# Kernel optimization log

Measured on AMD Instinct MI355X. Metric: run time of the kernel, lower is better.

The kernel has to match this reference:

```python
import jax, jax.numpy as jnp
import numpy as np

D_MODEL = 1024
NUM_HEADS = 16
KEY_DIM = 64
VALUE_DIM = 64
NEG_INF = jnp.float32(-1e30)


def setup_inputs() -> dict:
    key = jax.random.key(0)
    ks = jax.random.split(key, 10)
    B, S = 2, 2048
    lim = 1.0 / np.sqrt(D_MODEL)
    x = jax.random.normal(ks[0], (B, S, D_MODEL), dtype=jnp.float32)
    mask = jnp.ones((B, S), dtype=jnp.int32)  # pad mask: 1 = keep
    # stacked per-head linear params (Linear stores weight as [out, in])
    Wq = jax.random.uniform(ks[1], (NUM_HEADS, KEY_DIM, D_MODEL), jnp.float32, -lim, lim)
    bq = jax.random.uniform(ks[2], (NUM_HEADS, KEY_DIM), jnp.float32, -lim, lim)
    Wk = jax.random.uniform(ks[3], (NUM_HEADS, KEY_DIM, D_MODEL), jnp.float32, -lim, lim)
    bk = jax.random.uniform(ks[4], (NUM_HEADS, KEY_DIM), jnp.float32, -lim, lim)
    Wv = jax.random.uniform(ks[5], (NUM_HEADS, VALUE_DIM, D_MODEL), jnp.float32, -lim, lim)
    bv = jax.random.uniform(ks[6], (NUM_HEADS, VALUE_DIM), jnp.float32, -lim, lim)
    lim_o = 1.0 / np.sqrt(NUM_HEADS * VALUE_DIM)
    Wo = jax.random.uniform(ks[7], (D_MODEL, NUM_HEADS * VALUE_DIM), jnp.float32, -lim_o, lim_o)
    bo = jax.random.uniform(ks[8], (D_MODEL,), jnp.float32, -lim_o, lim_o)
    return {"x": x, "mask": mask, "Wq": Wq, "bq": bq, "Wk": Wk, "bk": bk,
            "Wv": Wv, "bv": bv, "Wo": Wo, "bo": bo}


def _mha(x, mask, Wq, bq, Wk, bk, Wv, bv, Wo, bo):
    B, S, _ = x.shape
    # per-head projections: [B, H, S, k]
    q = jnp.einsum('bsd,hkd->bhsk', x, Wq) + bq[None, :, None, :]
    k = jnp.einsum('bsd,hkd->bhsk', x, Wk) + bk[None, :, None, :]
    v = jnp.einsum('bsd,hvd->bhsv', x, Wv) + bv[None, :, None, :]
    scale = 1.0 / np.sqrt(KEY_DIM).astype(np.float32)
    scores = jnp.einsum('bhik,bhjk->bhij', q, k) * scale  # [B, H, S, S]
    # final mask = causal AND pad-row AND pad-col
    causal = jnp.tril(jnp.ones((S, S), dtype=bool))
    pad = mask.astype(bool)
    final = causal[None, None] & pad[:, None, :, None] & pad[:, None, None, :]
    masked = jnp.where(final, scores, NEG_INF)
    w = jax.nn.softmax(masked, axis=-1)
    w = jnp.where(final, w, 0.0)  # fully-masked rows -> zeros, matching loop impl
    out = jnp.einsum('bhij,bhjv->bhiv', w, v)            # [B, H, S, V]
    concat = out.transpose(0, 2, 1, 3).reshape(B, S, NUM_HEADS * VALUE_DIM)
    return concat @ Wo.T + bo


def reference(x, mask, Wq, bq, Wk, bk, Wv, bv, Wo, bo):
    return _mha(x, mask, Wq, bq, Wk, bk, Wv, bv, Wo, bo)
```

## Files before the change

kernel.cpp:

```cpp
#include <hip/hip_runtime.h>

#define SEQ 2048
#define NH 16
#define HD 64
#define DMODEL 1024

__device__ __forceinline__ unsigned int f2bf(float f) {
  unsigned int u = __float_as_uint(f);
  return ((u + 0x7fffu + ((u >> 16) & 1u)) >> 16) & 0xffffu;
}

__device__ __forceinline__ unsigned int pk2bf(float a, float b) {
  unsigned short ua = __builtin_bit_cast(unsigned short, (__bf16)a);
  unsigned short ub = __builtin_bit_cast(unsigned short, (__bf16)b);
  return (unsigned int)ua | ((unsigned int)ub << 16);
}

typedef __bf16 bf16x8 __attribute__((ext_vector_type(8)));
typedef float f32x4 __attribute__((ext_vector_type(4)));
typedef unsigned int uix4 __attribute__((ext_vector_type(4)));
typedef unsigned int uix2 __attribute__((ext_vector_type(2)));

__device__ __forceinline__ void gl2lds16(const unsigned short* g, unsigned short* l) {
  __builtin_amdgcn_global_load_lds(
      (const __attribute__((address_space(1))) unsigned int*)g,
      (__attribute__((address_space(3))) unsigned int*)l, 16, 0, 0);
}

__global__ __launch_bounds__(256) void cast_all_kernel(
    const float* __restrict__ x, const float* __restrict__ wq,
    const float* __restrict__ wk, const float* __restrict__ wv,
    const float* __restrict__ wo,
    unsigned short* __restrict__ xb, unsigned short* __restrict__ wqb,
    unsigned short* __restrict__ wkb, unsigned short* __restrict__ wvb,
    unsigned short* __restrict__ wob) {
  int idx = blockIdx.x * 256 + threadIdx.x;
  if (idx >= 1048576) return;
  const float* src;
  unsigned short* dst;
  int off;
  if (idx < 524288) {
    src = x; dst = xb; off = idx;
  } else {
    int t = idx - 524288;
    int w = t >> 17;
    off = t & 131071;
    src = (w == 0) ? wq : (w == 1) ? wk : (w == 2) ? wv : wo;
    dst = (w == 0) ? wqb : (w == 1) ? wkb : (w == 2) ? wvb : wob;
  }
  const float4* p = reinterpret_cast<const float4*>(src) + (size_t)off * 2;
  float4 a = p[0], b = p[1];
  uint4 o;
  o.x = f2bf(a.x) | (f2bf(a.y) << 16);
  o.y = f2bf(a.z) | (f2bf(a.w) << 16);
  o.z = f2bf(b.x) | (f2bf(b.y) << 16);
  o.w = f2bf(b.z) | (f2bf(b.w) << 16);
  reinterpret_cast<uint4*>(dst)[off] = o;
}

template <int MODE, int TM>
__global__ __launch_bounds__(256) void gemm128(
    const unsigned short* __restrict__ A, const unsigned short* __restrict__ B,
    const float* __restrict__ bias0, const float* __restrict__ bias1,
    const float* __restrict__ bias2, float* __restrict__ Cf,
    unsigned short* __restrict__ Qo, unsigned short* __restrict__ Ko,
    unsigned short* __restrict__ Vto, int Kdim) {
  constexpr int MT = TM / 32;
  __shared__ __align__(16) unsigned short As[2][TM * 64];
  __shared__ __align__(16) unsigned short Bs[2][128 * 64];
  const int tid = threadIdx.x;
  const int wave = tid >> 6, lane = tid & 63;
  const int wm = wave >> 1, wn = wave & 1;
  const int fr = lane & 15, quad = lane >> 4;
  const int fx = fr & 7;
  const int n0 = blockIdx.x * 128, m0 = blockIdx.y * TM;

  const int srowg = lane >> 3;
  const int schunk = (lane & 7) ^ (srowg & 7);
  const unsigned short* Abase =
      A + (size_t)(m0 + wave * (TM / 4) + srowg) * Kdim + schunk * 8;
  const unsigned short* Bbase =
      B + (size_t)(n0 + wave * 32 + srowg) * Kdim + schunk * 8;
  const int awoff = (wave * (TM / 4)) * 64;
  const int bwoff = (wave * 32) * 64;

  f32x4 acc[MT][4];
#pragma unroll
  for (int mt = 0; mt < MT; ++mt)
#pragma unroll
    for (int nt = 0; nt < 4; ++nt) acc[mt][nt] = f32x4{0.f, 0.f, 0.f, 0.f};

#pragma unroll
  for (int t = 0; t < TM / 32; ++t)
    gl2lds16(Abase + (size_t)(t * 8) * Kdim, As[0] + awoff + t * 8 * 64);
#pragma unroll
  for (int t = 0; t < 4; ++t)
    gl2lds16(Bbase + (size_t)(t * 8) * Kdim, Bs[0] + bwoff + t * 8 * 64);

  const int nk = Kdim >> 6;
  for (int kk = 0; kk < nk; ++kk) {
    __syncthreads();
    if (kk + 1 < nk) {
      const int k0n = (kk + 1) * 64;
      unsigned short* An = As[(kk + 1) & 1] + awoff;
      unsigned short* Bn = Bs[(kk + 1) & 1] + bwoff;
#pragma unroll
      for (int t = 0; t < TM / 32; ++t)
        gl2lds16(Abase + (size_t)(t * 8) * Kdim + k0n, An + t * 8 * 64);
#pragma unroll
      for (int t = 0; t < 4; ++t)
        gl2lds16(Bbase + (size_t)(t * 8) * Kdim + k0n, Bn + t * 8 * 64);
    }
    const unsigned short* Acur = As[kk & 1];
    const unsigned short* Bcur = Bs[kk & 1];
#pragma unroll
    for (int ks = 0; ks < 2; ++ks) {
      bf16x8 af[MT], bfv[4];
#pragma unroll
      for (int mt = 0; mt < MT; ++mt)
        af[mt] = *reinterpret_cast<const bf16x8*>(
            Acur + (wm * (TM / 2) + mt * 16 + fr) * 64 + ((ks * 4 + quad) ^ fx) * 8);
#pragma unroll
      for (int nt = 0; nt < 4; ++nt)
        bfv[nt] = *reinterpret_cast<const bf16x8*>(
            Bcur + (wn * 64 + nt * 16 + fr) * 64 + ((ks * 4 + quad) ^ fx) * 8);
#pragma unroll
      for (int mt = 0; mt < MT; ++mt)
#pragma unroll
        for (int nt = 0; nt < 4; ++nt)
          acc[mt][nt] = __builtin_amdgcn_mfma_f32_16x16x32_bf16(
              af[mt], bfv[nt], acc[mt][nt], 0, 0, 0);
    }
  }

  if (MODE == 0) {
    const int seg = n0 >> 10;
    const float* bp = (seg == 0) ? bias0 : (seg == 1) ? bias1 : bias2;
    const float scale = (seg == 0) ? 0.1803368809f : 1.0f;
    unsigned short* QK = (seg == 0) ? Qo : Ko;
#pragma unroll
    for (int nt = 0; nt < 4; ++nt) {
      const int c = (n0 + wn * 64 + nt * 16 + fr) & 1023;
      const int h = c >> 6, d = c & 63;
      const float bs = bp[c];
#pragma unroll
      for (int mt = 0; mt < MT; ++mt) {
        const int mbase = m0 + wm * (TM / 2) + mt * 16 + quad * 4;
        const int b = mbase >> 11, s0 = mbase & 2047;
        if (seg < 2) {
          unsigned short* dst = QK + (((size_t)(b * NH + h)) * SEQ + s0) * HD + d;
#pragma unroll
          for (int r = 0; r < 4; ++r)
            dst[(size_t)r * HD] = (unsigned short)f2bf((acc[mt][nt][r] + bs) * scale);
        } else {
          uint2 pk;
          pk.x = pk2bf(acc[mt][nt][0] + bs, acc[mt][nt][1] + bs);
          pk.y = pk2bf(acc[mt][nt][2] + bs, acc[mt][nt][3] + bs);
          *reinterpret_cast<uint2*>(
              Vto + (((size_t)(b * NH + h)) * HD + d) * SEQ + s0) = pk;
        }
      }
    }
  } else {
#pragma unroll
    for (int nt = 0; nt < 4; ++nt) {
      const int cg = n0 + wn * 64 + nt * 16 + fr;
      const float bs = bias0[cg];
#pragma unroll
      for (int mt = 0; mt < MT; ++mt) {
        const int mbase = m0 + wm * (TM / 2) + mt * 16 + quad * 4;
#pragma unroll
        for (int r = 0; r < 4; ++r)
          Cf[(size_t)(mbase + r) * DMODEL + cg] = acc[mt][nt][r] + bs;
      }
    }
  }
}

__global__ __launch_bounds__(256, 4) void attn_mfma_kernel(
    const unsigned short* __restrict__ Qg, const unsigned short* __restrict__ Kg,
    const unsigned short* __restrict__ Vtg, const int* __restrict__ mask,
    unsigned short* __restrict__ concat) {
  const int w = blockIdx.x >> 8;
  const int c = blockIdx.x & 255;
  const int gg = c >> 5;
  const int bh = c & 31;
  const int ib = (w == 0) ? (31 - gg) : (w == 1) ? gg : (w == 2) ? (23 - gg) : (8 + gg);
  const int b = bh >> 4, h = bh & 15;
  const int tid = threadIdx.x;
  const int wave = tid >> 6, lane = tid & 63;
  const int quad = lane >> 4, fr = lane & 15;
  const int fx = fr & 7;

  __shared__ __align__(16) unsigned short Ks[2][64 * 64];
  __shared__ __align__(16) unsigned short Vts[2][64 * 64];

  const unsigned short* Qb = Qg + ((size_t)bh * SEQ) * HD;
  const unsigned short* Kb = Kg + ((size_t)bh * SEQ) * HD;
  const unsigned short* Vtb = Vtg + ((size_t)bh * HD) * SEQ;
  const int* maskb = mask + b * SEQ;

  bool badl = false;
  {
    const int4* mp4 = reinterpret_cast<const int4*>(maskb);
#pragma unroll
    for (int u = 0; u < 8; ++u) {
      int4 v = mp4[lane * 8 + u];
      badl |= !(v.x && v.y && v.z && v.w);
    }
  }
  const unsigned long long bm = __ballot(badl);

  const int ir = ib * 64 + wave * 16 + fr;
  const bf16x8 q0 = *reinterpret_cast<const bf16x8*>(Qb + (size_t)ir * HD + quad * 8);
  const bf16x8 q1 = *reinterpret_cast<const bf16x8*>(Qb + (size_t)ir * HD + quad * 8 + 32);
  const int padi = maskb[ir];

  f32x4 o[4];
#pragma unroll
  for (int vt = 0; vt < 4; ++vt) o[vt] = f32x4{0.f, 0.f, 0.f, 0.f};
  float mr = -1e20f;
  float lq = 0.f;

  const int srow8 = lane >> 3;
  const int sch8 = (lane & 7) ^ (srow8 & 7);
  const int kprow = (wave >> 1) * 32 + ((srow8 >> 2)) * 8 + (wave & 1) * 4 + (srow8 & 3);
  const unsigned short* Kcol = Kb + sch8 * 8;
  const unsigned short* Vsrc = Vtb + (size_t)(wave * 16 + srow8) * SEQ + sch8 * 8;
  const int cA0 = (quad ^ fx) * 8;
  const int cA1 = ((quad + 4) ^ fx) * 8;

  {
    unsigned short* KsW = Ks[0] + (wave * 16) * 64;
    unsigned short* VtsW = Vts[0] + (wave * 16) * 64;
#pragma unroll
    for (int t = 0; t < 2; ++t) {
      gl2lds16(Kcol + (size_t)(kprow + t * 16) * HD, KsW + t * 8 * 64);
      gl2lds16(Vsrc + (size_t)(t * 8) * SEQ, VtsW + t * 8 * 64);
    }
  }

  for (int jc = 0; jc <= ib; ++jc) {
    __syncthreads();
    if (jc < ib) {
      const int jn = (jc + 1) * 64;
      unsigned short* KsW = Ks[(jc + 1) & 1] + (wave * 16) * 64;
      unsigned short* VtsW = Vts[(jc + 1) & 1] + (wave * 16) * 64;
#pragma unroll
      for (int t = 0; t < 2; ++t) {
        gl2lds16(Kcol + (size_t)(jn + kprow + t * 16) * HD, KsW + t * 8 * 64);
        gl2lds16(Vsrc + (size_t)(t * 8) * SEQ + jn, VtsW + t * 8 * 64);
      }
    }
    const unsigned short* Kcur = Ks[jc & 1];
    const unsigned short* Vcur = Vts[jc & 1];
    const int j0 = jc * 64;
    const bool tb = ((bm >> (2 * jc)) & 3ull) != 0ull;

    f32x4 st[4];
    __builtin_amdgcn_s_setprio(1);
#pragma unroll
    for (int jt = 0; jt < 4; ++jt) {
      bf16x8 ka0 = *reinterpret_cast<const bf16x8*>(&Kcur[(jt * 16 + fr) * 64 + cA0]);
      bf16x8 ka1 = *reinterpret_cast<const bf16x8*>(&Kcur[(jt * 16 + fr) * 64 + cA1]);
      st[jt] = f32x4{0.f, 0.f, 0.f, 0.f};
      st[jt] = __builtin_amdgcn_mfma_f32_16x16x32_bf16(ka0, q0, st[jt], 0, 0, 0);
      st[jt] = __builtin_amdgcn_mfma_f32_16x16x32_bf16(ka1, q1, st[jt], 0, 0, 0);
    }
    __builtin_amdgcn_s_setprio(0);

    if (tb) {
      const int4* mp = reinterpret_cast<const int4*>(maskb + j0);
#pragma unroll
      for (int jt = 0; jt < 4; ++jt) {
        const int4 mv = mp[(jt >> 1) * 8 + quad * 2 + (jt & 1)];
        if (mv.x == 0) st[jt][0] = -1e30f;
        if (mv.y == 0) st[jt][1] = -1e30f;
        if (mv.z == 0) st[jt][2] = -1e30f;
        if (mv.w == 0) st[jt][3] = -1e30f;
      }
    }
    if (jc == ib) {
#pragma unroll
      for (int jt = 0; jt < 4; ++jt) {
        const int jb = j0 + (jt >> 1) * 32 + quad * 8 + (jt & 1) * 4;
#pragma unroll
        for (int r = 0; r < 4; ++r)
          if (jb + r > ir) st[jt][r] = -1e30f;
      }
    }

    float tmax = -1e30f;
#pragma unroll
    for (int jt = 0; jt < 4; ++jt)
#pragma unroll
      for (int r = 0; r < 4; ++r) tmax = fmaxf(tmax, st[jt][r]);
    tmax = fmaxf(tmax, __shfl_xor(tmax, 16));
    {
      uix2 rr = __builtin_amdgcn_permlane32_swap(__float_as_uint(tmax),
                                                 __float_as_uint(tmax), false, false);
      tmax = fmaxf(__uint_as_float(rr.x), __uint_as_float(rr.y));
    }
    if (jc == 0) mr = fmaxf(tmax, -1e20f);

    unsigned int pw[8];
#pragma unroll
    for (int jt = 0; jt < 4; ++jt) {
      float p0 = __builtin_amdgcn_exp2f(fminf(st[jt][0] - mr, 60.f));
      float p1 = __builtin_amdgcn_exp2f(fminf(st[jt][1] - mr, 60.f));
      float p2 = __builtin_amdgcn_exp2f(fminf(st[jt][2] - mr, 60.f));
      float p3 = __builtin_amdgcn_exp2f(fminf(st[jt][3] - mr, 60.f));
      lq += (p0 + p1) + (p2 + p3);
      pw[2 * jt] = pk2bf(p0, p1);
      pw[2 * jt + 1] = pk2bf(p2, p3);
    }
    const bf16x8 pa0 = __builtin_bit_cast(bf16x8, uix4{pw[0], pw[1], pw[2], pw[3]});
    const bf16x8 pa1 = __builtin_bit_cast(bf16x8, uix4{pw[4], pw[5], pw[6], pw[7]});

    __builtin_amdgcn_s_setprio(1);
#pragma unroll
    for (int vt = 0; vt < 4; ++vt) {
      bf16x8 vb0 = *reinterpret_cast<const bf16x8*>(&Vcur[(vt * 16 + fr) * 64 + cA0]);
      bf16x8 vb1 = *reinterpret_cast<const bf16x8*>(&Vcur[(vt * 16 + fr) * 64 + cA1]);
      o[vt] = __builtin_amdgcn_mfma_f32_16x16x32_bf16(vb0, pa0, o[vt], 0, 0, 0);
      o[vt] = __builtin_amdgcn_mfma_f32_16x16x32_bf16(vb1, pa1, o[vt], 0, 0, 0);
    }
    __builtin_amdgcn_s_setprio(0);

    if (jc > 0) {
      const bool upd = __ballot(tmax > mr + 8.f) != 0ull;
      if (upd) {
        const float mn = fmaxf(mr, tmax);
        const float corr = __builtin_amdgcn_exp2f(mr - mn);
        mr = mn;
        lq *= corr;
#pragma unroll
        for (int vt = 0; vt < 4; ++vt) {
          o[vt][0] *= corr; o[vt][1] *= corr; o[vt][2] *= corr; o[vt][3] *= corr;
        }
      }
    }
  }

  float lr = lq;
  lr += __shfl_xor(lr, 16);
  lr += __shfl_xor(lr, 32);
  const float inv = (padi != 0 && lr > 0.f) ? 1.f / lr : 0.f;
  unsigned short* orow = concat + ((size_t)(b * SEQ + ir)) * DMODEL + h * HD;
#pragma unroll
  for (int vt = 0; vt < 4; ++vt) {
    uint2 pk;
    pk.x = pk2bf(o[vt][0] * inv, o[vt][1] * inv);
    pk.y = pk2bf(o[vt][2] * inv, o[vt][3] * inv);
    *reinterpret_cast<uint2*>(orow + vt * 16 + quad * 4) = pk;
  }
}

extern "C" void kernel_launch(void* const* d_in, const int* in_sizes, int n_in,
                              void* d_out, int out_size, void* d_ws, size_t ws_size,
                              hipStream_t stream) {
  (void)in_sizes; (void)n_in; (void)out_size;
  const float* x  = (const float*)d_in[0];
  const int* mask = (const int*)d_in[1];
  const float* Wq = (const float*)d_in[2];
  const float* bq = (const float*)d_in[3];
  const float* Wk = (const float*)d_in[4];
  const float* bk = (const float*)d_in[5];
  const float* Wv = (const float*)d_in[6];
  const float* bv = (const float*)d_in[7];
  const float* Wo = (const float*)d_in[8];
  const float* bo = (const float*)d_in[9];
  float* out = (float*)d_out;

  char* ws = (char*)d_ws;
  if (ws_size < (48ull << 20)) return;
  unsigned short* xb  = (unsigned short*)(ws);
  unsigned short* wqb = (unsigned short*)(ws + (8ull  << 20));
  unsigned short* wkb = (unsigned short*)(ws + (10ull << 20));
  unsigned short* wvb = (unsigned short*)(ws + (12ull << 20));
  unsigned short* wob = (unsigned short*)(ws + (14ull << 20));
  unsigned short* Qb  = (unsigned short*)(ws + (16ull << 20));
  unsigned short* Kb  = (unsigned short*)(ws + (24ull << 20));
  unsigned short* Vtb = (unsigned short*)(ws + (32ull << 20));
  unsigned short* cb  = (unsigned short*)(ws + (40ull << 20));

  cast_all_kernel<<<4096, 256, 0, stream>>>(x, Wq, Wk, Wv, Wo, xb, wqb, wkb, wvb, wob);

  gemm128<0, 128><<<dim3(24, 32), 256, 0, stream>>>(xb, wqb, bq, bk, bv,
                                                    nullptr, Qb, Kb, Vtb, 1024);

  attn_mfma_kernel<<<1024, 256, 0, stream>>>(Qb, Kb, Vtb, mask, cb);

  gemm128<1, 64><<<dim3(8, 64), 256, 0, stream>>>(cb, wob, bo, nullptr, nullptr,
                                                  out, nullptr, nullptr, nullptr, 1024);
}
```

Baseline: 192.6 us.

## Process two 16-row query tiles per wave in attention with 128-thread blocks

The attention kernel now uses 2 waves per block instead of 4, and each wave handles 32 query rows as two 16-row tiles. Every K and V fragment read from LDS therefore feeds two MFMAs. Each wave also issues twice as many global-to-LDS loads to fill the same 64x64 tiles. This cuts LDS read traffic per MFMA and gives each wave more independent work. The cost is roughly double the register use per wave for accumulators and scores, fewer waves per block, and a rescale that now triggers for both row tiles whenever either one needs it.

Result: slower. 204.7 us (+6.3%).

```diff
diff --git a/kernel.cpp b/kernel.cpp
--- a/kernel.cpp
+++ b/kernel.cpp
@@ -177,7 +177,7 @@
   }
 }
 
-__global__ __launch_bounds__(256, 4) void attn_mfma_kernel(
+__global__ __launch_bounds__(128, 3) void attn_mfma_kernel(
     const unsigned short* __restrict__ Qg, const unsigned short* __restrict__ Kg,
     const unsigned short* __restrict__ Vtg, const int* __restrict__ mask,
     unsigned short* __restrict__ concat) {
@@ -211,45 +211,49 @@
   }
   const unsigned long long bm = __ballot(badl);
 
-  const int ir = ib * 64 + wave * 16 + fr;
-  const bf16x8 q0 = *reinterpret_cast<const bf16x8*>(Qb + (size_t)ir * HD + quad * 8);
-  const bf16x8 q1 = *reinterpret_cast<const bf16x8*>(Qb + (size_t)ir * HD + quad * 8 + 32);
-  const int padi = maskb[ir];
-
-  f32x4 o[4];
-#pragma unroll
-  for (int vt = 0; vt < 4; ++vt) o[vt] = f32x4{0.f, 0.f, 0.f, 0.f};
-  float mr = -1e20f;
-  float lq = 0.f;
-
-  const int srow8 = lane >> 3;
-  const int sch8 = (lane & 7) ^ (srow8 & 7);
-  const int kprow = (wave >> 1) * 32 + ((srow8 >> 2)) * 8 + (wave & 1) * 4 + (srow8 & 3);
-  const unsigned short* Kcol = Kb + sch8 * 8;
-  const unsigned short* Vsrc = Vtb + (size_t)(wave * 16 + srow8) * SEQ + sch8 * 8;
+  int ir[2], padi[2];
+  bf16x8 q[2][2];
+#pragma unroll
+  for (int it = 0; it < 2; ++it) {
+    ir[it] = ib * 64 + wave * 32 + it * 16 + fr;
+    q[it][0] = *reinterpret_cast<const bf16x8*>(Qb + (size_t)ir[it] * HD + quad * 8);
+    q[it][1] = *reinterpret_cast<const bf16x8*>(Qb + (size_t)ir[it] * HD + quad * 8 + 32);
+    padi[it] = maskb[ir[it]];
+  }
+
+  f32x4 o[2][4];
+#pragma unroll
+  for (int it = 0; it < 2; ++it)
+#pragma unroll
+    for (int vt = 0; vt < 4; ++vt) o[it][vt] = f32x4{0.f, 0.f, 0.f, 0.f};
+  float mr[2] = {-1e20f, -1e20f};
+  float lq[2] = {0.f, 0.f};
+
+  const int sr = lane >> 3;
+  const int sch = (lane & 7) ^ (sr & 7);
+  const unsigned short* Kcol = Kb + sch * 8;
+  const unsigned short* Vsrc = Vtb + (size_t)(wave * 32 + sr) * SEQ + sch * 8;
   const int cA0 = (quad ^ fx) * 8;
   const int cA1 = ((quad + 4) ^ fx) * 8;
 
-  {
-    unsigned short* KsW = Ks[0] + (wave * 16) * 64;
-    unsigned short* VtsW = Vts[0] + (wave * 16) * 64;
-#pragma unroll
-    for (int t = 0; t < 2; ++t) {
-      gl2lds16(Kcol + (size_t)(kprow + t * 16) * HD, KsW + t * 8 * 64);
-      gl2lds16(Vsrc + (size_t)(t * 8) * SEQ, VtsW + t * 8 * 64);
-    }
+#pragma unroll
+  for (int t = 0; t < 4; ++t) {
+    const int kp = wave * 32 + ((t & 1) << 4) + ((sr >> 2) << 3) + ((t >> 1) << 2) + (sr & 3);
+    gl2lds16(Kcol + (size_t)kp * HD, Ks[0] + (wave * 32 + t * 8) * 64);
+    gl2lds16(Vsrc + (size_t)(t * 8) * SEQ, Vts[0] + (wave * 32 + t * 8) * 64);
   }
 
   for (int jc = 0; jc <= ib; ++jc) {
     __syncthreads();
     if (jc < ib) {
       const int jn = (jc + 1) * 64;
-      unsigned short* KsW = Ks[(jc + 1) & 1] + (wave * 16) * 64;
-      unsigned short* VtsW = Vts[(jc + 1) & 1] + (wave * 16) * 64;
-#pragma unroll
-      for (int t = 0; t < 2; ++t) {
-        gl2lds16(Kcol + (size_t)(jn + kprow + t * 16) * HD, KsW + t * 8 * 64);
-        gl2lds16(Vsrc + (size_t)(t * 8) * SEQ + jn, VtsW + t * 8 * 64);
+      unsigned short* Ksn = Ks[(jc + 1) & 1];
+      unsigned short* Vtsn = Vts[(jc + 1) & 1];
+#pragma unroll
+      for (int t = 0; t < 4; ++t) {
+        const int kp = wave * 32 + ((t & 1) << 4) + ((sr >> 2) << 3) + ((t >> 1) << 2) + (sr & 3);
+        gl2lds16(Kcol + (size_t)(jn + kp) * HD, Ksn + (wave * 32 + t * 8) * 64);
+        gl2lds16(Vsrc + (size_t)(t * 8) * SEQ + jn, Vtsn + (wave * 32 + t * 8) * 64);
       }
     }
     const unsigned short* Kcur = Ks[jc & 1];
@@ -257,15 +261,18 @@
     const int j0 = jc * 64;
     const bool tb = ((bm >> (2 * jc)) & 3ull) != 0ull;
 
-    f32x4 st[4];
+    f32x4 st[2][4];
     __builtin_amdgcn_s_setprio(1);
 #pragma unroll
     for (int jt = 0; jt < 4; ++jt) {
       bf16x8 ka0 = *reinterpret_cast<const bf16x8*>(&Kcur[(jt * 16 + fr) * 64 + cA0]);
       bf16x8 ka1 = *reinterpret_cast<const bf16x8*>(&Kcur[(jt * 16 + fr) * 64 + cA1]);
-      st[jt] = f32x4{0.f, 0.f, 0.f, 0.f};
-      st[jt] = __builtin_amdgcn_mfma_f32_16x16x32_bf16(ka0, q0, st[jt], 0, 0, 0);
-      st[jt] = __builtin_amdgcn_mfma_f32_16x16x32_bf16(ka1, q1, st[jt], 0, 0, 0);
+#pragma unroll
+      for (int it = 0; it < 2; ++it) {
+        st[it][jt] = f32x4{0.f, 0.f, 0.f, 0.f};
+        st[it][jt] = __builtin_amdgcn_mfma_f32_16x16x32_bf16(ka0, q[it][0], st[it][jt], 0, 0, 0);
+        st[it][jt] = __builtin_amdgcn_mfma_f32_16x16x32_bf16(ka1, q[it][1], st[it][jt], 0, 0, 0);
+      }
     }
     __builtin_amdgcn_s_setprio(0);
 
@@ -274,10 +281,13 @@
 #pragma unroll
       for (int jt = 0; jt < 4; ++jt) {
         const int4 mv = mp[(jt >> 1) * 8 + quad * 2 + (jt & 1)];
-        if (mv.x == 0) st[jt][0] = -1e30f;
-        if (mv.y == 0) st[jt][1] = -1e30f;
-        if (mv.z == 0) st[jt][2] = -1e30f;
-        if (mv.w == 0) st[jt][3] = -1e30f;
+#pragma unroll
+        for (int it = 0; it < 2; ++it) {
+          if (mv.x == 0) st[it][jt][0] = -1e30f;
+          if (mv.y == 0) st[it][jt][1] = -1e30f;
+          if (mv.z == 0) st[it][jt][2] = -1e30f;
+          if (mv.w == 0) st[it][jt][3] = -1e30f;
+        }
       }
     }
     if (jc == ib) {
@@ -285,74 +295,95 @@
       for (int jt = 0; jt < 4; ++jt) {
         const int jb = j0 + (jt >> 1) * 32 + quad * 8 + (jt & 1) * 4;
 #pragma unroll
-        for (int r = 0; r < 4; ++r)
-          if (jb + r > ir) st[jt][r] = -1e30f;
-      }
-    }
-
-    float tmax = -1e30f;
-#pragma unroll
-    for (int jt = 0; jt < 4; ++jt)
-#pragma unroll
-      for (int r = 0; r < 4; ++r) tmax = fmaxf(tmax, st[jt][r]);
-    tmax = fmaxf(tmax, __shfl_xor(tmax, 16));
-    {
-      uix2 rr = __builtin_amdgcn_permlane32_swap(__float_as_uint(tmax),
-                                                 __float_as_uint(tmax), false, false);
-      tmax = fmaxf(__uint_as_float(rr.x), __uint_as_float(rr.y));
-    }
-    if (jc == 0) mr = fmaxf(tmax, -1e20f);
-
-    unsigned int pw[8];
-#pragma unroll
-    for (int jt = 0; jt < 4; ++jt) {
-      float p0 = __builtin_amdgcn_exp2f(fminf(st[jt][0] - mr, 60.f));
-      float p1 = __builtin_amdgcn_exp2f(fminf(st[jt][1] - mr, 60.f));
-      float p2 = __builtin_amdgcn_exp2f(fminf(st[jt][2] - mr, 60.f));
-      float p3 = __builtin_amdgcn_exp2f(fminf(st[jt][3] - mr, 60.f));
-      lq += (p0 + p1) + (p2 + p3);
-      pw[2 * jt] = pk2bf(p0, p1);
-      pw[2 * jt + 1] = pk2bf(p2, p3);
-    }
-    const bf16x8 pa0 = __builtin_bit_cast(bf16x8, uix4{pw[0], pw[1], pw[2], pw[3]});
-    const bf16x8 pa1 = __builtin_bit_cast(bf16x8, uix4{pw[4], pw[5], pw[6], pw[7]});
+        for (int it = 0; it < 2; ++it)
+#pragma unroll
+          for (int r = 0; r < 4; ++r)
+            if (jb + r > ir[it]) st[it][jt][r] = -1e30f;
+      }
+    }
+
+    float tmax[2];
+#pragma unroll
+    for (int it = 0; it < 2; ++it) {
+      float t0 = -1e30f;
+#pragma unroll
+      for (int jt = 0; jt < 4; ++jt)
+#pragma unroll
+        for (int r = 0; r < 4; ++r) t0 = fmaxf(t0, st[it][jt][r]);
+      t0 = fmaxf(t0, __shfl_xor(t0, 16));
+      uix2 rr = __builtin_amdgcn_permlane32_swap(__float_as_uint(t0),
+                                                 __float_as_uint(t0), false, false);
+      tmax[it] = fmaxf(__uint_as_float(rr.x), __uint_as_float(rr.y));
+    }
+    if (jc == 0) {
+      mr[0] = fmaxf(tmax[0], -1e20f);
+      mr[1] = fmaxf(tmax[1], -1e20f);
+    }
+
+    bf16x8 pa[2][2];
+#pragma unroll
+    for (int it = 0; it < 2; ++it) {
+      unsigned int pw[8];
+#pragma unroll
+      for (int jt = 0; jt < 4; ++jt) {
+        float p0 = __builtin_amdgcn_exp2f(fminf(st[it][jt][0] - mr[it], 60.f));
+        float p1 = __builtin_amdgcn_exp2f(fminf(st[it][jt][1] - mr[it], 60.f));
+        float p2 = __builtin_amdgcn_exp2f(fminf(st[it][jt][2] - mr[it], 60.f));
+        float p3 = __builtin_amdgcn_exp2f(fminf(st[it][jt][3] - mr[it], 60.f));
+        lq[it] += (p0 + p1) + (p2 + p3);
+        pw[2 * jt] = pk2bf(p0, p1);
+        pw[2 * jt + 1] = pk2bf(p2, p3);
+      }
+      pa[it][0] = __builtin_bit_cast(bf16x8, uix4{pw[0], pw[1], pw[2], pw[3]});
+      pa[it][1] = __builtin_bit_cast(bf16x8, uix4{pw[4], pw[5], pw[6], pw[7]});
+    }
 
     __builtin_amdgcn_s_setprio(1);
 #pragma unroll
     for (int vt = 0; vt < 4; ++vt) {
       bf16x8 vb0 = *reinterpret_cast<const bf16x8*>(&Vcur[(vt * 16 + fr) * 64 + cA0]);
       bf16x8 vb1 = *reinterpret_cast<const bf16x8*>(&Vcur[(vt * 16 + fr) * 64 + cA1]);
-      o[vt] = __builtin_amdgcn_mfma_f32_16x16x32_bf16(vb0, pa0, o[vt], 0, 0, 0);
-      o[vt] = __builtin_amdgcn_mfma_f32_16x16x32_bf16(vb1, pa1, o[vt], 0, 0, 0);
+#pragma unroll
+      for (int it = 0; it < 2; ++it) {
+        o[it][vt] = __builtin_amdgcn_mfma_f32_16x16x32_bf16(vb0, pa[it][0], o[it][vt], 0, 0, 0);
+        o[it][vt] = __builtin_amdgcn_mfma_f32_16x16x32_bf16(vb1, pa[it][1], o[it][vt], 0, 0, 0);
+      }
     }
     __builtin_amdgcn_s_setprio(0);
 
     if (jc > 0) {
-      const bool upd = __ballot(tmax > mr + 8.f) != 0ull;
-      if (upd) {
-        const float mn = fmaxf(mr, tmax);
-        const float corr = __builtin_amdgcn_exp2f(mr - mn);
-        mr = mn;
-        lq *= corr;
-#pragma unroll
-        for (int vt = 0; vt < 4; ++vt) {
-          o[vt][0] *= corr; o[vt][1] *= corr; o[vt][2] *= corr; o[vt][3] *= corr;
+      const bool need = (tmax[0] > mr[0] + 8.f) || (tmax[1] > mr[1] + 8.f);
+      if (__ballot(need) != 0ull) {
+#pragma unroll
+        for (int it = 0; it < 2; ++it) {
+          const float mn = fmaxf(mr[it], tmax[it]);
+          const float corr = __builtin_amdgcn_exp2f(mr[it] - mn);
+          mr[it] = mn;
+          lq[it] *= corr;
+#pragma unroll
+          for (int vt = 0; vt < 4; ++vt) {
+            o[it][vt][0] *= corr; o[it][vt][1] *= corr;
+            o[it][vt][2] *= corr; o[it][vt][3] *= corr;
+          }
         }
       }
     }
   }
 
-  float lr = lq;
-  lr += __shfl_xor(lr, 16);
-  lr += __shfl_xor(lr, 32);
-  const float inv = (padi != 0 && lr > 0.f) ? 1.f / lr : 0.f;
-  unsigned short* orow = concat + ((size_t)(b * SEQ + ir)) * DMODEL + h * HD;
-#pragma unroll
-  for (int vt = 0; vt < 4; ++vt) {
-    uint2 pk;
-    pk.x = pk2bf(o[vt][0] * inv, o[vt][1] * inv);
-    pk.y = pk2bf(o[vt][2] * inv, o[vt][3] * inv);
-    *reinterpret_cast<uint2*>(orow + vt * 16 + quad * 4) = pk;
+#pragma unroll
+  for (int it = 0; it < 2; ++it) {
+    float lr = lq[it];
+    lr += __shfl_xor(lr, 16);
+    lr += __shfl_xor(lr, 32);
+    const float inv = (padi[it] != 0 && lr > 0.f) ? 1.f / lr : 0.f;
+    unsigned short* orow = concat + ((size_t)(b * SEQ + ir[it])) * DMODEL + h * HD;
+#pragma unroll
+    for (int vt = 0; vt < 4; ++vt) {
+      uint2 pk;
+      pk.x = pk2bf(o[it][vt][0] * inv, o[it][vt][1] * inv);
+      pk.y = pk2bf(o[it][vt][2] * inv, o[it][vt][3] * inv);
+      *reinterpret_cast<uint2*>(orow + vt * 16 + quad * 4) = pk;
+    }
   }
 }
 
@@ -389,7 +420,7 @@
   gemm128<0, 128><<<dim3(24, 32), 256, 0, stream>>>(xb, wqb, bq, bk, bv,
                                                     nullptr, Qb, Kb, Vtb, 1024);
 
-  attn_mfma_kernel<<<1024, 256, 0, stream>>>(Qb, Kb, Vtb, mask, cb);
+  attn_mfma_kernel<<<1024, 128, 0, stream>>>(Qb, Kb, Vtb, mask, cb);
 
   gemm128<1, 64><<<dim3(8, 64), 256, 0, stream>>>(cb, wob, bo, nullptr, nullptr,
                                                   out, nullptr, nullptr, nullptr, 1024);
```

## Replace QKV projection GEMM with 256x256 eight-wave phased pipelined kernel

Applied to the files above, without the earlier changes.

Adds a dedicated QKV projection kernel that uses 256x256 output tiles with 8 waves, double-buffered LDS loaded via direct global-to-LDS copies, and an eight-phase schedule that interleaves staging of the next K-slice with MFMA on the current one using barriers, vmcnt waits and setprio. The aim is to raise arithmetic intensity per block and hide global memory latency behind MFMA compute compared with the previous 128x128 generic GEMM. The grid shrinks to 192 blocks of 512 threads with 128 KB of shared memory, which may underfill the GPU's compute units and limit occupancy. The bias, Q scaling and Q/K/Vt layout epilogue are carried over.

Result: slower. 197.7 us (+2.6%).

```diff
diff --git a/kernel.cpp b/kernel.cpp
--- a/kernel.cpp
+++ b/kernel.cpp
@@ -58,6 +58,140 @@
   reinterpret_cast<uint4*>(dst)[off] = o;
 }
 
+__global__ __launch_bounds__(512, 2) void gemm8ph_qkv(
+    const unsigned short* __restrict__ A, const unsigned short* __restrict__ B,
+    const float* __restrict__ bias0, const float* __restrict__ bias1,
+    const float* __restrict__ bias2,
+    unsigned short* __restrict__ Qo, unsigned short* __restrict__ Ko,
+    unsigned short* __restrict__ Vto) {
+  constexpr int KD = 1024;
+  __shared__ __align__(16) unsigned short Asl[2][256 * 64];
+  __shared__ __align__(16) unsigned short Bsl[2][256 * 64];
+  const int tid = threadIdx.x;
+  const int wave = tid >> 6, lane = tid & 63;
+  const int wm = wave >> 2, wn = wave & 3;
+  const int fr = lane & 15, quad = lane >> 4;
+  const int fx = fr & 7;
+  const int n0 = blockIdx.x * 256, m0 = blockIdx.y * 256;
+
+  const int sr = lane >> 3;
+  const int sch = (lane & 7) ^ (sr & 7);
+  const unsigned short* Ab = A + (size_t)(m0 + wave * 8 + sr) * KD + sch * 8;
+  const unsigned short* Bb = B + (size_t)(n0 + wave * 8 + sr) * KD + sch * 8;
+
+  f32x4 acc[8][4];
+#pragma unroll
+  for (int mt = 0; mt < 8; ++mt)
+#pragma unroll
+    for (int nt = 0; nt < 4; ++nt) acc[mt][nt] = f32x4{0.f, 0.f, 0.f, 0.f};
+
+#define G8_STAGE_A(slot, h, k0)                                         \
+  do {                                                                  \
+    gl2lds16(Ab + (size_t)((h) * 128) * KD + (k0),                      \
+             &Asl[slot][((h) * 128 + wave * 8) * 64]);                  \
+    gl2lds16(Ab + (size_t)((h) * 128 + 64) * KD + (k0),                 \
+             &Asl[slot][((h) * 128 + 64 + wave * 8) * 64]);             \
+  } while (0)
+#define G8_STAGE_B(slot, h, k0)                                         \
+  do {                                                                  \
+    gl2lds16(Bb + (size_t)((h) * 128) * KD + (k0),                      \
+             &Bsl[slot][((h) * 128 + wave * 8) * 64]);                  \
+    gl2lds16(Bb + (size_t)((h) * 128 + 64) * KD + (k0),                 \
+             &Bsl[slot][((h) * 128 + 64 + wave * 8) * 64]);             \
+  } while (0)
+#define G8_READ(s, mq, nq)                                              \
+  bf16x8 af[4][2], bfv[2][2];                                           \
+  _Pragma("unroll") for (int f = 0; f < 4; ++f)                         \
+  _Pragma("unroll") for (int ks = 0; ks < 2; ++ks)                      \
+      af[f][ks] = *reinterpret_cast<const bf16x8*>(                     \
+          &Asl[s][(wm * 128 + ((mq)*4 + f) * 16 + fr) * 64 +            \
+                  ((ks * 4 + quad) ^ fx) * 8]);                         \
+  _Pragma("unroll") for (int g = 0; g < 2; ++g)                         \
+  _Pragma("unroll") for (int ks = 0; ks < 2; ++ks)                      \
+      bfv[g][ks] = *reinterpret_cast<const bf16x8*>(                    \
+          &Bsl[s][(wn * 64 + ((nq)*2 + g) * 16 + fr) * 64 +             \
+                  ((ks * 4 + quad) ^ fx) * 8]);
+#define G8_MMA(mq, nq)                                                  \
+  __builtin_amdgcn_s_setprio(1);                                        \
+  _Pragma("unroll") for (int ks = 0; ks < 2; ++ks)                      \
+  _Pragma("unroll") for (int f = 0; f < 4; ++f)                         \
+  _Pragma("unroll") for (int g = 0; g < 2; ++g)                         \
+      acc[(mq)*4 + f][(nq)*2 + g] =                                     \
+          __builtin_amdgcn_mfma_f32_16x16x32_bf16(                      \
+              af[f][ks], bfv[g][ks], acc[(mq)*4 + f][(nq)*2 + g], 0, 0, 0); \
+  __builtin_amdgcn_s_setprio(0);
+#define G8_BAR asm volatile("s_barrier" ::: "memory")
+#define G8_VM2 asm volatile("s_waitcnt vmcnt(2)" ::: "memory")
+
+  G8_STAGE_A(0, 0, 0); G8_STAGE_A(0, 1, 0);
+  G8_STAGE_B(0, 0, 0); G8_STAGE_B(0, 1, 0);
+
+  for (int j = 0; j < 8; ++j) {
+    const int kB = j * 128 + 64;
+    const int kC = j * 128 + 128;
+    {
+      G8_STAGE_A(1, 0, kB); G8_VM2; G8_BAR;
+      G8_READ(0, 0, 0) G8_MMA(0, 0) G8_BAR;
+    }
+    {
+      G8_READ(0, 0, 1) G8_STAGE_A(1, 1, kB); G8_BAR; G8_MMA(0, 1) G8_BAR;
+    }
+    {
+      G8_READ(0, 1, 0) G8_STAGE_B(1, 0, kB); G8_BAR; G8_MMA(1, 0) G8_BAR;
+    }
+    {
+      G8_READ(0, 1, 1) G8_STAGE_B(1, 1, kB); G8_BAR; G8_MMA(1, 1) G8_BAR;
+    }
+    {
+      G8_STAGE_A(0, 0, kC); G8_VM2; G8_BAR;
+      G8_READ(1, 0, 0) G8_MMA(0, 0) G8_BAR;
+    }
+    {
+      G8_READ(1, 0, 1) G8_STAGE_A(0, 1, kC); G8_BAR; G8_MMA(0, 1) G8_BAR;
+    }
+    {
+      G8_READ(1, 1, 0) G8_STAGE_B(0, 0, kC); G8_BAR; G8_MMA(1, 0) G8_BAR;
+    }
+    {
+      G8_READ(1, 1, 1) G8_STAGE_B(0, 1, kC); G8_BAR; G8_MMA(1, 1) G8_BAR;
+    }
+  }
+
+  const int seg = n0 >> 10;
+  const float* bp = (seg == 0) ? bias0 : (seg == 1) ? bias1 : bias2;
+  const float scale = (seg == 0) ? 0.1803368809f : 1.0f;
+  unsigned short* QK = (seg == 0) ? Qo : Ko;
+#pragma unroll
+  for (int nt = 0; nt < 4; ++nt) {
+    const int c = (n0 + wn * 64 + nt * 16 + fr) & 1023;
+    const int h = c >> 6, d = c & 63;
+    const float bs = bp[c];
+#pragma unroll
+    for (int mt = 0; mt < 8; ++mt) {
+      const int mbase = m0 + wm * 128 + mt * 16 + quad * 4;
+      const int b = mbase >> 11, s0 = mbase & 2047;
+      if (seg < 2) {
+        unsigned short* dst = QK + (((size_t)(b * NH + h)) * SEQ + s0) * HD + d;
+#pragma unroll
+        for (int r = 0; r < 4; ++r)
+          dst[(size_t)r * HD] = (unsigned short)f2bf((acc[mt][nt][r] + bs) * scale);
+      } else {
+        uint2 pk;
+        pk.x = pk2bf(acc[mt][nt][0] + bs, acc[mt][nt][1] + bs);
+        pk.y = pk2bf(acc[mt][nt][2] + bs, acc[mt][nt][3] + bs);
+        *reinterpret_cast<uint2*>(
+            Vto + (((size_t)(b * NH + h)) * HD + d) * SEQ + s0) = pk;
+      }
+    }
+  }
+#undef G8_STAGE_A
+#undef G8_STAGE_B
+#undef G8_READ
+#undef G8_MMA
+#undef G8_BAR
+#undef G8_VM2
+}
+
 template <int MODE, int TM>
 __global__ __launch_bounds__(256) void gemm128(
     const unsigned short* __restrict__ A, const unsigned short* __restrict__ B,
@@ -386,8 +520,7 @@
 
   cast_all_kernel<<<4096, 256, 0, stream>>>(x, Wq, Wk, Wv, Wo, xb, wqb, wkb, wvb, wob);
 
-  gemm128<0, 128><<<dim3(24, 32), 256, 0, stream>>>(xb, wqb, bq, bk, bv,
-                                                    nullptr, Qb, Kb, Vtb, 1024);
+  gemm8ph_qkv<<<dim3(12, 16), 512, 0, stream>>>(xb, wqb, bq, bk, bv, Qb, Kb, Vtb);
 
   attn_mfma_kernel<<<1024, 256, 0, stream>>>(Qb, Kb, Vtb, mask, cb);
 
```

## Split long causal attention rows across two blocks and merge partials

Applied to the files above, without the earlier changes.

Query blocks 20–31, which have the longest causal key ranges, are now split into two key-range halves handled by separate blocks. Each half writes unnormalized partial outputs plus row max and row sum to workspace. A new combine kernel merges the pairs with log-sum-exp rescaling. A table-driven schedule orders the work units longest-first, and the occupancy hint rises from 4 to 5 blocks per SM. The aim is to cut the tail of the causal load imbalance, at the cost of an extra launch, fp32 partial traffic, and reuse of workspace regions that held earlier bf16 buffers.

New measurement: 202.4 us. 1.05x slower.

```diff
diff --git a/kernel.cpp b/kernel.cpp
--- a/kernel.cpp
+++ b/kernel.cpp
@@ -177,15 +177,19 @@
   }
 }
 
-__global__ __launch_bounds__(256, 4) void attn_mfma_kernel(
+__device__ const int ATT_IB[44] = {19,18,17,16,15,30,31,31,14,28,29,29,30,13,26,27,27,28,12,24,25,25,26,11,22,23,23,24,10,20,21,21,22, 9,20, 8, 7, 6, 5, 4, 3, 2, 1, 0};
+__device__ const int ATT_LO[44] = { 0, 0, 0, 0, 0, 0, 0,16, 0, 0, 0,15,16, 0, 0, 0,14,15, 0, 0, 0,13,14, 0, 0, 0,12,13, 0, 0, 0,11,12, 0,11, 0, 0, 0, 0, 0, 0, 0, 0, 0};
+__device__ const int ATT_HI[44] = {19,18,17,16,15,15,15,31,14,14,14,29,30,13,13,13,27,28,12,12,12,25,26,11,11,11,23,24,10,10,10,21,22, 9,20, 8, 7, 6, 5, 4, 3, 2, 1, 0};
+__device__ const int ATT_HF[44] = {-1,-1,-1,-1,-1, 0, 0, 1,-1, 0, 0, 1, 1,-1, 0, 0, 1, 1,-1, 0, 0, 1, 1,-1, 0, 0, 1, 1,-1, 0, 0, 1, 1,-1, 1,-1,-1,-1,-1,-1,-1,-1,-1,-1};
+
+__global__ __launch_bounds__(256, 5) void attn_mfma_kernel(
     const unsigned short* __restrict__ Qg, const unsigned short* __restrict__ Kg,
     const unsigned short* __restrict__ Vtg, const int* __restrict__ mask,
-    unsigned short* __restrict__ concat) {
-  const int w = blockIdx.x >> 8;
-  const int c = blockIdx.x & 255;
-  const int gg = c >> 5;
-  const int bh = c & 31;
-  const int ib = (w == 0) ? (31 - gg) : (w == 1) ? gg : (w == 2) ? (23 - gg) : (8 + gg);
+    unsigned short* __restrict__ concat,
+    float* __restrict__ part_o, float* __restrict__ part_ml) {
+  const int u = blockIdx.x >> 5;
+  const int bh = blockIdx.x & 31;
+  const int ib = ATT_IB[u], jlo = ATT_LO[u], jhi = ATT_HI[u], hf = ATT_HF[u];
   const int b = bh >> 4, h = bh & 15;
   const int tid = threadIdx.x;
   const int wave = tid >> 6, lane = tid & 63;
@@ -204,8 +208,8 @@
   {
     const int4* mp4 = reinterpret_cast<const int4*>(maskb);
 #pragma unroll
-    for (int u = 0; u < 8; ++u) {
-      int4 v = mp4[lane * 8 + u];
+    for (int uu = 0; uu < 8; ++uu) {
+      int4 v = mp4[lane * 8 + uu];
       badl |= !(v.x && v.y && v.z && v.w);
     }
   }
@@ -231,18 +235,19 @@
   const int cA1 = ((quad + 4) ^ fx) * 8;
 
   {
-    unsigned short* KsW = Ks[0] + (wave * 16) * 64;
-    unsigned short* VtsW = Vts[0] + (wave * 16) * 64;
+    const int jl64 = jlo * 64;
+    unsigned short* KsW = Ks[jlo & 1] + (wave * 16) * 64;
+    unsigned short* VtsW = Vts[jlo & 1] + (wave * 16) * 64;
 #pragma unroll
     for (int t = 0; t < 2; ++t) {
-      gl2lds16(Kcol + (size_t)(kprow + t * 16) * HD, KsW + t * 8 * 64);
-      gl2lds16(Vsrc + (size_t)(t * 8) * SEQ, VtsW + t * 8 * 64);
-    }
-  }
-
-  for (int jc = 0; jc <= ib; ++jc) {
+      gl2lds16(Kcol + (size_t)(jl64 + kprow + t * 16) * HD, KsW + t * 8 * 64);
+      gl2lds16(Vsrc + (size_t)(t * 8) * SEQ + jl64, VtsW + t * 8 * 64);
+    }
+  }
+
+  for (int jc = jlo; jc <= jhi; ++jc) {
     __syncthreads();
-    if (jc < ib) {
+    if (jc < jhi) {
       const int jn = (jc + 1) * 64;
       unsigned short* KsW = Ks[(jc + 1) & 1] + (wave * 16) * 64;
       unsigned short* VtsW = Vts[(jc + 1) & 1] + (wave * 16) * 64;
@@ -301,7 +306,7 @@
                                                  __float_as_uint(tmax), false, false);
       tmax = fmaxf(__uint_as_float(rr.x), __uint_as_float(rr.y));
     }
-    if (jc == 0) mr = fmaxf(tmax, -1e20f);
+    if (jc == jlo) mr = fmaxf(tmax, -1e20f);
 
     unsigned int pw[8];
 #pragma unroll
@@ -327,7 +332,7 @@
     }
     __builtin_amdgcn_s_setprio(0);
 
-    if (jc > 0) {
+    if (jc > jlo) {
       const bool upd = __ballot(tmax > mr + 8.f) != 0ull;
       if (upd) {
         const float mn = fmaxf(mr, tmax);
@@ -345,15 +350,65 @@
   float lr = lq;
   lr += __shfl_xor(lr, 16);
   lr += __shfl_xor(lr, 32);
-  const float inv = (padi != 0 && lr > 0.f) ? 1.f / lr : 0.f;
-  unsigned short* orow = concat + ((size_t)(b * SEQ + ir)) * DMODEL + h * HD;
-#pragma unroll
-  for (int vt = 0; vt < 4; ++vt) {
-    uint2 pk;
-    pk.x = pk2bf(o[vt][0] * inv, o[vt][1] * inv);
-    pk.y = pk2bf(o[vt][2] * inv, o[vt][3] * inv);
-    *reinterpret_cast<uint2*>(orow + vt * 16 + quad * 4) = pk;
-  }
+
+  if (hf < 0) {
+    const float inv = (padi != 0 && lr > 0.f) ? 1.f / lr : 0.f;
+    unsigned short* orow = concat + ((size_t)(b * SEQ + ir)) * DMODEL + h * HD;
+#pragma unroll
+    for (int vt = 0; vt < 4; ++vt) {
+      uint2 pk;
+      pk.x = pk2bf(o[vt][0] * inv, o[vt][1] * inv);
+      pk.y = pk2bf(o[vt][2] * inv, o[vt][3] * inv);
+      *reinterpret_cast<uint2*>(orow + vt * 16 + quad * 4) = pk;
+    }
+  } else {
+    const int entry = (bh * 12 + (ib - 20)) * 2 + hf;
+    float* po = part_o + ((size_t)entry * 64 + (wave * 16 + fr)) * 64;
+#pragma unroll
+    for (int vt = 0; vt < 4; ++vt)
+      *reinterpret_cast<f32x4*>(po + vt * 16 + quad * 4) = o[vt];
+    if (quad == 0) {
+      float* pml = part_ml + (size_t)entry * 128;
+      pml[wave * 16 + fr] = mr;
+      pml[64 + wave * 16 + fr] = lr;
+    }
+  }
+}
+
+__global__ __launch_bounds__(256) void attn_combine_kernel(
+    const float* __restrict__ part_o, const float* __restrict__ part_ml,
+    const int* __restrict__ mask, unsigned short* __restrict__ concat) {
+  const int bx = blockIdx.x;
+  const int bh = bx / 12, q = bx % 12;
+  const int ib = 20 + q;
+  const int b = bh >> 4, h = bh & 15;
+  const int r = threadIdx.x >> 2, cg = threadIdx.x & 3;
+  const int e0 = (bh * 12 + q) * 2;
+  const float m1 = part_ml[(size_t)e0 * 128 + r];
+  const float l1 = part_ml[(size_t)e0 * 128 + 64 + r];
+  const float m2 = part_ml[(size_t)(e0 + 1) * 128 + r];
+  const float l2 = part_ml[(size_t)(e0 + 1) * 128 + 64 + r];
+  const float m = fmaxf(m1, m2);
+  const float c1 = __builtin_amdgcn_exp2f(m1 - m);
+  const float c2 = __builtin_amdgcn_exp2f(m2 - m);
+  const float l = l1 * c1 + l2 * c2;
+  const int i = ib * 64 + r;
+  const int padi = mask[b * SEQ + i];
+  const float inv = (padi != 0 && l > 0.f) ? 1.f / l : 0.f;
+  const float s1 = c1 * inv, s2 = c2 * inv;
+  const float* po1 = part_o + ((size_t)e0 * 64 + r) * 64 + cg * 16;
+  const float* po2 = part_o + ((size_t)(e0 + 1) * 64 + r) * 64 + cg * 16;
+  unsigned int wb[8];
+#pragma unroll
+  for (int v = 0; v < 4; ++v) {
+    f32x4 a = *reinterpret_cast<const f32x4*>(po1 + v * 4);
+    f32x4 c = *reinterpret_cast<const f32x4*>(po2 + v * 4);
+    wb[2 * v] = pk2bf(a[0] * s1 + c[0] * s2, a[1] * s1 + c[1] * s2);
+    wb[2 * v + 1] = pk2bf(a[2] * s1 + c[2] * s2, a[3] * s1 + c[3] * s2);
+  }
+  unsigned short* dst = concat + ((size_t)(b * SEQ + i)) * DMODEL + h * HD + cg * 16;
+  reinterpret_cast<uint4*>(dst)[0] = uint4{wb[0], wb[1], wb[2], wb[3]};
+  reinterpret_cast<uint4*>(dst)[1] = uint4{wb[4], wb[5], wb[6], wb[7]};
 }
 
 extern "C" void kernel_launch(void* const* d_in, const int* in_sizes, int n_in,
@@ -383,13 +438,16 @@
   unsigned short* Kb  = (unsigned short*)(ws + (24ull << 20));
   unsigned short* Vtb = (unsigned short*)(ws + (32ull << 20));
   unsigned short* cb  = (unsigned short*)(ws + (40ull << 20));
+  float* part_o  = (float*)(ws);
+  float* part_ml = (float*)(ws + (13ull << 20));
 
   cast_all_kernel<<<4096, 256, 0, stream>>>(x, Wq, Wk, Wv, Wo, xb, wqb, wkb, wvb, wob);
 
   gemm128<0, 128><<<dim3(24, 32), 256, 0, stream>>>(xb, wqb, bq, bk, bv,
                                                     nullptr, Qb, Kb, Vtb, 1024);
 
-  attn_mfma_kernel<<<1024, 256, 0, stream>>>(Qb, Kb, Vtb, mask, cb);
+  attn_mfma_kernel<<<1408, 256, 0, stream>>>(Qb, Kb, Vtb, mask, cb, part_o, part_ml);
+  attn_combine_kernel<<<384, 256, 0, stream>>>(part_o, part_ml, mask, cb);
 
   gemm128<1, 64><<<dim3(8, 64), 256, 0, stream>>>(cb, wob, bo, nullptr, nullptr,
                                                   out, nullptr, nullptr, nullptr, 1024);
```
